# Kernel optimization log

Measured on AMD Instinct MI355X. Metric: run time of the kernel, lower is better.

## Reference

```python
import jax, jax.numpy as jnp
import numpy as np

B, S, H = 1, 2048, 2048
NH, HD, RD = 32, 64, 64      # n_heads, head_dim, qk_mqa_dim (rope dim)
QR, KVR = 1024, 896          # q_lora_rank, kv_lora_rank
EPS = 1e-6
SCALE = HD ** -0.5           # scaling = head_dim ** -0.5 (as in module)


def rotate_half(x):
    x1, x2 = jnp.split(x, 2, axis=-1)
    return jnp.concatenate((-x2, x1), axis=-1)


def rmsnorm(x, w):
    var = jnp.mean(jnp.square(x), axis=-1, keepdims=True)
    return x * jax.lax.rsqrt(var + EPS) * w


def setup_inputs() -> dict:
    key = jax.random.key(0)
    ks = jax.random.split(key, 8)
    hidden_states = jax.random.normal(ks[0], (B, S, H), jnp.float32)
    # rotary tables over RD dims (applied only to the rope slice)
    inv_freq = 1.0 / (10000.0 ** (np.arange(0, RD, 2, dtype=np.float32) / RD))
    ang = np.arange(S, dtype=np.float32)[:, None] * inv_freq[None, :]
    emb = np.concatenate([ang, ang], axis=-1)  # [S, RD]
    cos = jnp.tile(jnp.asarray(np.cos(emb))[None], (B, 1, 1))
    sin = jnp.tile(jnp.asarray(np.sin(emb))[None], (B, 1, 1))
    s = 0.02
    q_a_w = s * jax.random.normal(ks[1], (QR, H), jnp.float32)
    q_a_ln_w = jnp.ones((QR,), jnp.float32)
    q_b_w = s * jax.random.normal(ks[2], (NH * (HD + RD), QR), jnp.float32)
    kv_a_w = s * jax.random.normal(ks[3], (KVR + RD, H), jnp.float32)
    kv_a_ln_w = jnp.ones((KVR,), jnp.float32)
    kv_b_w = s * jax.random.normal(ks[4], (NH * 2 * HD, KVR), jnp.float32)
    o_w = s * jax.random.normal(ks[5], (H, NH * HD), jnp.float32)
    return {"hidden_states": hidden_states, "cos": cos, "sin": sin,
            "q_a_w": q_a_w, "q_a_ln_w": q_a_ln_w, "q_b_w": q_b_w,
            "kv_a_w": kv_a_w, "kv_a_ln_w": kv_a_ln_w, "kv_b_w": kv_b_w,
            "o_w": o_w}


def reference(hidden_states, cos, sin, q_a_w, q_a_ln_w, q_b_w,
              kv_a_w, kv_a_ln_w, kv_b_w, o_w):
    b, s, _ = hidden_states.shape
    # Q: low-rank down -> RMSNorm -> up, split nope/rope per head
    q_lat = rmsnorm(hidden_states @ q_a_w.T, q_a_ln_w)             # [B,S,QR]
    q = (q_lat @ q_b_w.T).reshape(b, s, NH, HD + RD).transpose(0, 2, 1, 3)
    q_nope, q_rope = q[..., :HD], q[..., HD:]                      # [B,NH,S,HD/RD]
    # KV: joint down-proj with shared MQA rope key
    ckv = hidden_states @ kv_a_w.T                                 # [B,S,KVR+RD]
    c_kv, k_rope = ckv[..., :KVR], ckv[..., KVR:]
    k_rope = k_rope[:, None]                                       # [B,1,S,RD]
    kv = (rmsnorm(c_kv, kv_a_ln_w) @ kv_b_w.T).reshape(b, s, NH, 2 * HD)
    kv = kv.transpose(0, 2, 1, 3)                                  # [B,NH,S,2HD]
    k_nope, v = kv[..., :HD], kv[..., HD:]
    # RoPE on rope slices only (cos/sin unsqueezed over head dim)
    c_, s_ = cos[:, None], sin[:, None]
    q_rope = q_rope * c_ + rotate_half(q_rope) * s_
    k_rope = k_rope * c_ + rotate_half(k_rope) * s_
    q_full = jnp.concatenate([q_nope, q_rope], axis=-1)            # [B,NH,S,HD+RD]
    k_full = jnp.concatenate(
        [k_nope, jnp.broadcast_to(k_rope, (b, NH, s, RD))], axis=-1)
    # causal SDPA
    scores = jnp.einsum('bhqd,bhkd->bhqk', q_full, k_full) * SCALE
    mask = jnp.tril(jnp.ones((s, s), bool))
    scores = jnp.where(mask, scores, jnp.finfo(scores.dtype).min)
    attn = jax.nn.softmax(scores, axis=-1)
    out = jnp.einsum('bhqk,bhkd->bhqd', attn, v)                   # [B,NH,S,HD]
    out = out.transpose(0, 2, 1, 3).reshape(b, s, NH * HD)
    return out @ o_w.T                                             # [B,S,H]
```

## Files before the change

kernel.cpp:

```cpp
#include <hip/hip_runtime.h>


typedef __attribute__((ext_vector_type(8))) __bf16 bf16x8;
typedef __attribute__((ext_vector_type(4))) float f32x4;
typedef __attribute__((ext_vector_type(4))) unsigned u32x4;

__device__ __forceinline__ unsigned short f2bf(float f) {
  unsigned int x = __builtin_bit_cast(unsigned int, f);
  x += 0x7fffu + ((x >> 16) & 1u);
  return (unsigned short)(x >> 16);
}
__device__ __forceinline__ float bf2f(unsigned short u) {
  unsigned int x = ((unsigned int)u) << 16;
  return __builtin_bit_cast(float, x);
}
__device__ __forceinline__ void gload_lds16(const void* g, void* l) {
  __builtin_amdgcn_global_load_lds(
      (const __attribute__((address_space(1))) void*)g,
      (__attribute__((address_space(3))) void*)l, 16, 0, 0);
}
__device__ __forceinline__ void cstore(float* C, size_t i, float v) { C[i] = v; }
__device__ __forceinline__ void cstore(unsigned short* C, size_t i, float v) { C[i] = f2bf(v); }

struct CvtSegs {
  const float* src[6];
  unsigned short* dst[6];
  unsigned int n_src[6];
  unsigned int n_tot[6];
  unsigned int blk0[7];
};

__global__ __launch_bounds__(256) void cvt_all(CvtSegs sg) {
  int b = blockIdx.x;
  int seg = 0;
#pragma unroll
  for (int k = 0; k < 5; ++k)
    if (b >= (int)sg.blk0[k + 1]) seg = k + 1;
  size_t i = ((size_t)(b - sg.blk0[seg]) * 256 + threadIdx.x) * 4;
  if (i >= sg.n_tot[seg]) return;
  unsigned short o0 = 0, o1 = 0, o2 = 0, o3 = 0;
  if (i < sg.n_src[seg]) {
    float4 v = *reinterpret_cast<const float4*>(sg.src[seg] + i);
    o0 = f2bf(v.x); o1 = f2bf(v.y); o2 = f2bf(v.z); o3 = f2bf(v.w);
  }
  *reinterpret_cast<ushort4*>(sg.dst[seg] + i) = make_ushort4(o0, o1, o2, o3);
}

template <typename OutT>
__global__ __launch_bounds__(512, 4) void gemm_bt2(const unsigned short* __restrict__ A,
                                                   const unsigned short* __restrict__ B,
                                                   OutT* __restrict__ C,
                                                   int M, int N, int K) {
  __shared__ unsigned short lA0[128 * 64], lA1[128 * 64];
  __shared__ unsigned short lB0[64 * 64], lB1[64 * 64];
  const int tid = threadIdx.x, lane = tid & 63, wv = tid >> 6;
  const int wr = wv >> 1, wc = wv & 1;

  unsigned nwg = gridDim.x * gridDim.y;
  unsigned lid = blockIdx.y * gridDim.x + blockIdx.x;
  unsigned swz_id = (lid & 7) * (nwg >> 3) + (lid >> 3);
  const int bm = (int)(swz_id / gridDim.x) * 128;
  const int bn = (int)(swz_id % gridDim.x) * 64;

  f32x4 acc[2][2] = {};

  const int ar0 = tid >> 3;
  const int acol = (((tid & 7) ^ ((tid >> 3) & 7))) * 8;
  const int swz = lane & 7;

  auto stage = [&](unsigned short* la, unsigned short* lb, int k0) {
#pragma unroll
    for (int i = 0; i < 2; ++i)
      gload_lds16(A + (size_t)(bm + i * 64 + ar0) * K + k0 + acol,
                  &la[(i * 512 + wv * 64) * 8]);
    gload_lds16(B + (size_t)(bn + ar0) * K + k0 + acol, &lb[(wv * 64) * 8]);
  };

  auto compute = [&](const unsigned short* la, const unsigned short* lb) {
#pragma unroll
    for (int ks = 0; ks < 2; ++ks) {
      const int ch = ((ks * 4 + (lane >> 4)) ^ swz) * 8;
      bf16x8 af[2], bfr[2];
#pragma unroll
      for (int m = 0; m < 2; ++m)
        af[m] = *reinterpret_cast<const bf16x8*>(
            &la[(wr * 32 + m * 16 + (lane & 15)) * 64 + ch]);
#pragma unroll
      for (int n = 0; n < 2; ++n)
        bfr[n] = *reinterpret_cast<const bf16x8*>(
            &lb[(wc * 32 + n * 16 + (lane & 15)) * 64 + ch]);
      __builtin_amdgcn_s_setprio(1);
#pragma unroll
      for (int m = 0; m < 2; ++m)
#pragma unroll
        for (int n = 0; n < 2; ++n)
          acc[m][n] = __builtin_amdgcn_mfma_f32_16x16x32_bf16(af[m], bfr[n], acc[m][n], 0, 0, 0);
      __builtin_amdgcn_s_setprio(0);
    }
  };

  stage(lA0, lB0, 0);
  for (int k0 = 0; k0 < K; k0 += 128) {
    __syncthreads();
    stage(lA1, lB1, k0 + 64);
    compute(lA0, lB0);
    __syncthreads();
    if (k0 + 128 < K) stage(lA0, lB0, k0 + 128);
    compute(lA1, lB1);
  }

  const int r0 = bm + wr * 32, c0 = bn + wc * 32;
#pragma unroll
  for (int m = 0; m < 2; ++m)
#pragma unroll
    for (int n = 0; n < 2; ++n)
#pragma unroll
      for (int r = 0; r < 4; ++r)
        cstore(C, (size_t)(r0 + m * 16 + (lane >> 4) * 4 + r) * N + c0 + n * 16 + (lane & 15),
               acc[m][n][r]);
}

__global__ __launch_bounds__(256) void rmsnorm_rope(const float* __restrict__ C1,
                                                    const float* __restrict__ qw,
                                                    const float* __restrict__ kvw,
                                                    const float* __restrict__ cosp,
                                                    const float* __restrict__ sinp,
                                                    unsigned short* __restrict__ qn,
                                                    unsigned short* __restrict__ ckvn,
                                                    unsigned short* __restrict__ kr) {
  const int s = blockIdx.x, tid = threadIdx.x;
  const float* row = C1 + (size_t)s * 2048;
  __shared__ float red[4];

  float4 v = *reinterpret_cast<const float4*>(row + tid * 4);
  float ss = v.x * v.x + v.y * v.y + v.z * v.z + v.w * v.w;
  ss += __shfl_xor(ss, 32); ss += __shfl_xor(ss, 16); ss += __shfl_xor(ss, 8);
  ss += __shfl_xor(ss, 4);  ss += __shfl_xor(ss, 2);  ss += __shfl_xor(ss, 1);
  if ((tid & 63) == 0) red[tid >> 6] = ss;
  __syncthreads();
  float rs = rsqrtf((red[0] + red[1] + red[2] + red[3]) * (1.f / 1024.f) + 1e-6f);
  {
    float4 w = *reinterpret_cast<const float4*>(qw + tid * 4);
    *reinterpret_cast<ushort4*>(qn + (size_t)s * 1024 + tid * 4) =
        make_ushort4(f2bf(v.x * rs * w.x), f2bf(v.y * rs * w.y),
                     f2bf(v.z * rs * w.z), f2bf(v.w * rs * w.w));
  }

  float4 u = make_float4(0.f, 0.f, 0.f, 0.f);
  if (tid < 224) u = *reinterpret_cast<const float4*>(row + 1024 + tid * 4);
  ss = u.x * u.x + u.y * u.y + u.z * u.z + u.w * u.w;
  ss += __shfl_xor(ss, 32); ss += __shfl_xor(ss, 16); ss += __shfl_xor(ss, 8);
  ss += __shfl_xor(ss, 4);  ss += __shfl_xor(ss, 2);  ss += __shfl_xor(ss, 1);
  __syncthreads();
  if ((tid & 63) == 0) red[tid >> 6] = ss;
  __syncthreads();
  rs = rsqrtf((red[0] + red[1] + red[2] + red[3]) * (1.f / 896.f) + 1e-6f);
  if (tid < 224) {
    float4 w = *reinterpret_cast<const float4*>(kvw + tid * 4);
    *reinterpret_cast<ushort4*>(ckvn + (size_t)s * 896 + tid * 4) =
        make_ushort4(f2bf(u.x * rs * w.x), f2bf(u.y * rs * w.y),
                     f2bf(u.z * rs * w.z), f2bf(u.w * rs * w.w));
  }

  if (tid < 64) {
    int d = tid;
    float x = row[1920 + d];
    float part = (d < 32) ? -row[1920 + d + 32] : row[1920 + d - 32];
    float vv = x * cosp[(size_t)s * 64 + d] + part * sinp[(size_t)s * 64 + d];
    kr[(size_t)s * 64 + d] = f2bf(vv);
  }
}

__global__ __launch_bounds__(256) void kv_post(const unsigned short* __restrict__ KVfb,
                                               unsigned short* __restrict__ Vt) {
  __shared__ unsigned short lT[64 * 65];
  const int s0 = blockIdx.x * 64, h = blockIdx.y, tid = threadIdx.x;
  for (int idx = tid; idx < 4096; idx += 256) {
    int r = idx >> 6, c = idx & 63;
    lT[r * 65 + c] = KVfb[(size_t)(s0 + r) * 4096 + h * 128 + 64 + c];
  }
  __syncthreads();
  for (int idx = tid; idx < 4096; idx += 256) {
    int d = idx >> 6, c = idx & 63;
    Vt[((size_t)h * 64 + d) * 2048 + s0 + c] = lT[c * 65 + d];
  }
}

__global__ __launch_bounds__(256, 4) void flash_attn(const unsigned short* __restrict__ Qfb,
                                                     const unsigned short* __restrict__ KVfb,
                                                     const unsigned short* __restrict__ kr,
                                                     const float* __restrict__ cosp,
                                                     const float* __restrict__ sinp,
                                                     const unsigned short* __restrict__ Vt,
                                                     float* __restrict__ Op,
                                                     float2* __restrict__ Ml) {
  __shared__ unsigned short lK0[64 * 128], lK1[64 * 128];
  const int tid = threadIdx.x, lane = tid & 63, wv = tid >> 6;
  const int h = blockIdx.x;
  const int qb = 31 - ((int)blockIdx.y >> 1);
  const int j = (int)blockIdx.y & 1;
  const int q0 = qb * 64;
  const int firstrow = q0 + wv * 16;
  const int g = lane >> 4;
  const int qa = firstrow + (lane & 15);
  const float SC = 0.18033688f;

  bf16x8 qf[4];
  {
    const unsigned short* qr = Qfb + (size_t)qa * 4096 + h * 128;
    float raw[4][8];
#pragma unroll
    for (int ks = 0; ks < 4; ++ks) {
      ushort4 u0 = *reinterpret_cast<const ushort4*>(qr + ks * 32 + g * 8);
      ushort4 u1 = *reinterpret_cast<const ushort4*>(qr + ks * 32 + g * 8 + 4);
      raw[ks][0] = bf2f(u0.x); raw[ks][1] = bf2f(u0.y);
      raw[ks][2] = bf2f(u0.z); raw[ks][3] = bf2f(u0.w);
      raw[ks][4] = bf2f(u1.x); raw[ks][5] = bf2f(u1.y);
      raw[ks][6] = bf2f(u1.z); raw[ks][7] = bf2f(u1.w);
    }
    const float* cp = cosp + (size_t)qa * 64 + g * 8;
    const float* sp = sinp + (size_t)qa * 64 + g * 8;
    float c0[8], s0[8], c1[8], s1[8];
    {
      float4 a = *reinterpret_cast<const float4*>(cp);
      float4 b = *reinterpret_cast<const float4*>(cp + 4);
      c0[0]=a.x;c0[1]=a.y;c0[2]=a.z;c0[3]=a.w;c0[4]=b.x;c0[5]=b.y;c0[6]=b.z;c0[7]=b.w;
      a = *reinterpret_cast<const float4*>(cp + 32);
      b = *reinterpret_cast<const float4*>(cp + 36);
      c1[0]=a.x;c1[1]=a.y;c1[2]=a.z;c1[3]=a.w;c1[4]=b.x;c1[5]=b.y;c1[6]=b.z;c1[7]=b.w;
      a = *reinterpret_cast<const float4*>(sp);
      b = *reinterpret_cast<const float4*>(sp + 4);
      s0[0]=a.x;s0[1]=a.y;s0[2]=a.z;s0[3]=a.w;s0[4]=b.x;s0[5]=b.y;s0[6]=b.z;s0[7]=b.w;
      a = *reinterpret_cast<const float4*>(sp + 32);
      b = *reinterpret_cast<const float4*>(sp + 36);
      s1[0]=a.x;s1[1]=a.y;s1[2]=a.z;s1[3]=a.w;s1[4]=b.x;s1[5]=b.y;s1[6]=b.z;s1[7]=b.w;
    }
    alignas(16) unsigned short pk[4][8];
#pragma unroll
    for (int e = 0; e < 8; ++e) {
      pk[0][e] = f2bf(raw[0][e] * SC);
      pk[1][e] = f2bf(raw[1][e] * SC);
      pk[2][e] = f2bf((raw[2][e] * c0[e] - raw[3][e] * s0[e]) * SC);
      pk[3][e] = f2bf((raw[3][e] * c1[e] + raw[2][e] * s1[e]) * SC);
    }
#pragma unroll
    for (int ks = 0; ks < 4; ++ks)
      qf[ks] = *reinterpret_cast<const bf16x8*>(pk[ks]);
  }

  f32x4 o_acc[4] = {};
  float mrow = -1e30f, lrow = 0.f;

  const int sl0 = ((g & 1) * 2) * 16 + (lane & 15);
  const int sl1 = sl0 + 16;
  const bool hi = g >= 2;

  const int krow = wv * 4 + (lane >> 4);
  const int cs = (lane & 15) ^ (krow & 7);
  const int swz = lane & 7;

  auto stage = [&](int t, unsigned short* lK) {
    int jj = t * 64;
#pragma unroll
    for (int i = 0; i < 4; ++i) {
      int s = jj + i * 16 + krow;
      const unsigned short* src =
          (cs < 8) ? KVfb + (size_t)s * 4096 + h * 128 + cs * 8
                   : kr + (size_t)s * 64 + (cs - 8) * 8;
      gload_lds16(src, &lK[(i * 16 + wv * 4) * 128]);
    }
  };

  auto loadV = [&](int j0, bf16x8 (&vr)[2][4]) {
#pragma unroll
    for (int ks = 0; ks < 2; ++ks)
#pragma unroll
      for (int n = 0; n < 4; ++n)
        vr[ks][n] = *reinterpret_cast<const bf16x8*>(
            Vt + ((size_t)h * 64 + n * 16 + (lane & 15)) * 2048 + j0 + ks * 32 +
            (lane >> 4) * 8);
  };

  auto computeT = [&](int j0, const unsigned short* lK, const bf16x8 (&vr)[2][4]) {
    f32x4 sT[4] = {};
    __builtin_amdgcn_s_setprio(1);
#pragma unroll
    for (int n = 0; n < 4; ++n)
#pragma unroll
      for (int ks = 0; ks < 4; ++ks) {
        bf16x8 kf = *reinterpret_cast<const bf16x8*>(
            &lK[(n * 16 + (lane & 15)) * 128 + (((ks * 4 + (lane >> 4)) ^ swz)) * 8]);
        sT[n] = __builtin_amdgcn_mfma_f32_16x16x32_bf16(kf, qf[ks], sT[n], 0, 0, 0);
      }
    __builtin_amdgcn_s_setprio(0);

    if (j0 == q0) {
#pragma unroll
      for (int n = 0; n < 4; ++n)
#pragma unroll
        for (int r = 0; r < 4; ++r) {
          int key = j0 + n * 16 + g * 4 + r;
          if (key > qa) sT[n][r] = -1e30f;
        }
    }

    float tm[4];
#pragma unroll
    for (int n = 0; n < 4; ++n)
      tm[n] = fmaxf(fmaxf(sT[n][0], sT[n][1]), fmaxf(sT[n][2], sT[n][3]));
    float mx = fmaxf(fmaxf(tm[0], tm[1]), fmaxf(tm[2], tm[3]));
    mx = fmaxf(mx, __shfl_xor(mx, 16));
    mx = fmaxf(mx, __shfl_xor(mx, 32));

    if (__any(mx - mrow > 8.0f)) {
      float mn = fmaxf(mrow, mx);
      float sf = exp2f(mrow - mn);
      mrow = mn;
      lrow *= sf;
      float sfr[4];
#pragma unroll
      for (int r = 0; r < 4; ++r) sfr[r] = __shfl(sf, (lane >> 4) * 4 + r);
#pragma unroll
      for (int n = 0; n < 4; ++n)
#pragma unroll
        for (int r = 0; r < 4; ++r) o_acc[n][r] *= sfr[r];
    }

    float psn[4];
    unsigned dw[4][2];
#pragma unroll
    for (int n = 0; n < 4; ++n) {
      float p0 = exp2f(sT[n][0] - mrow), p1 = exp2f(sT[n][1] - mrow);
      float p2 = exp2f(sT[n][2] - mrow), p3 = exp2f(sT[n][3] - mrow);
      psn[n] = (p0 + p1) + (p2 + p3);
      asm("v_cvt_pk_bf16_f32 %0, %1, %2" : "=v"(dw[n][0]) : "v"(p0), "v"(p1));
      asm("v_cvt_pk_bf16_f32 %0, %1, %2" : "=v"(dw[n][1]) : "v"(p2), "v"(p3));
    }
    float ps = (psn[0] + psn[1]) + (psn[2] + psn[3]);
    ps += __shfl_xor(ps, 16);
    ps += __shfl_xor(ps, 32);
    lrow += ps;

#pragma unroll
    for (int ks = 0; ks < 2; ++ks) {
      unsigned A0 = __shfl(dw[2 * ks][0], sl0);
      unsigned B0 = __shfl(dw[2 * ks + 1][0], sl0);
      unsigned A1 = __shfl(dw[2 * ks][1], sl0);
      unsigned B1 = __shfl(dw[2 * ks + 1][1], sl0);
      unsigned A2 = __shfl(dw[2 * ks][0], sl1);
      unsigned B2 = __shfl(dw[2 * ks + 1][0], sl1);
      unsigned A3 = __shfl(dw[2 * ks][1], sl1);
      unsigned B3 = __shfl(dw[2 * ks + 1][1], sl1);
      u32x4 mm;
      mm.x = hi ? B0 : A0; mm.y = hi ? B1 : A1;
      mm.z = hi ? B2 : A2; mm.w = hi ? B3 : A3;
      bf16x8 pa = __builtin_bit_cast(bf16x8, mm);
      __builtin_amdgcn_s_setprio(1);
#pragma unroll
      for (int n = 0; n < 4; ++n)
        o_acc[n] = __builtin_amdgcn_mfma_f32_16x16x32_bf16(pa, vr[ks][n], o_acc[n], 0, 0, 0);
      __builtin_amdgcn_s_setprio(0);
    }
  };

  bf16x8 vr[2][4];
  unsigned short* cur = lK0;
  unsigned short* nxt = lK1;
  if (j <= qb) stage(j, cur);
  for (int t = j; t <= qb; t += 2) {
    __syncthreads();
    if (t + 2 <= qb) stage(t + 2, nxt);
    loadV(t * 64, vr);
    computeT(t * 64, cur, vr);
    unsigned short* tmp = cur; cur = nxt; nxt = tmp;
  }

  float* op = Op + (size_t)j * 4194304 + ((size_t)h * 2048 + firstrow) * 64;
#pragma unroll
  for (int n = 0; n < 4; ++n)
#pragma unroll
    for (int r = 0; r < 4; ++r)
      op[(size_t)(g * 4 + r) * 64 + n * 16 + (lane & 15)] = o_acc[n][r];
  if (lane < 16)
    Ml[(size_t)j * 65536 + h * 2048 + qa] = make_float2(mrow, lrow);
}

__global__ __launch_bounds__(256) void flash_combine(const float* __restrict__ Op,
                                                     const float2* __restrict__ Ml,
                                                     unsigned short* __restrict__ Ao) {
  size_t i4 = ((size_t)blockIdx.x * 256 + threadIdx.x) * 4;
  int s = (int)(i4 >> 11);
  int c = (int)(i4 & 2047);
  int h = c >> 6, d = c & 63;
  float2 a = Ml[h * 2048 + s];
  float2 b = Ml[65536 + h * 2048 + s];
  float M = fmaxf(a.x, b.x);
  float w0 = exp2f(a.x - M), w1 = exp2f(b.x - M);
  float inv = 1.f / (w0 * a.y + w1 * b.y);
  size_t pidx = ((size_t)h * 2048 + s) * 64 + d;
  float4 o0 = *reinterpret_cast<const float4*>(Op + pidx);
  float4 o1 = *reinterpret_cast<const float4*>(Op + 4194304 + pidx);
  *reinterpret_cast<ushort4*>(Ao + (size_t)s * 2048 + h * 64 + d) =
      make_ushort4(f2bf((w0 * o0.x + w1 * o1.x) * inv),
                   f2bf((w0 * o0.y + w1 * o1.y) * inv),
                   f2bf((w0 * o0.z + w1 * o1.z) * inv),
                   f2bf((w0 * o0.w + w1 * o1.w) * inv));
}

extern "C" void kernel_launch(void* const* d_in, const int* in_sizes, int n_in,
                              void* d_out, int out_size, void* d_ws, size_t ws_size,
                              hipStream_t stream) {
  const float* hs   = (const float*)d_in[0];
  const float* cosp = (const float*)d_in[1];
  const float* sinp = (const float*)d_in[2];
  const float* qaw  = (const float*)d_in[3];
  const float* qaln = (const float*)d_in[4];
  const float* qbwf = (const float*)d_in[5];
  const float* kvaw = (const float*)d_in[6];
  const float* kvln = (const float*)d_in[7];
  const float* kvbwf= (const float*)d_in[8];
  const float* owf  = (const float*)d_in[9];
  float* out = (float*)d_out;
  char* ws = (char*)d_ws;
  const size_t MB = 1u << 20;

  unsigned short* W1b  = (unsigned short*)(ws + 0);
  unsigned short* Ao   = (unsigned short*)(ws + 0);
  unsigned short* qbw  = (unsigned short*)(ws + 8 * MB);
  unsigned short* Vt   = (unsigned short*)(ws + 8 * MB);
  unsigned short* kvbw = (unsigned short*)(ws + 16 * MB);
  unsigned short* owb  = (unsigned short*)(ws + 23 * MB);
  unsigned short* hsb  = (unsigned short*)(ws + 31 * MB);
  unsigned short* Qfb  = (unsigned short*)(ws + 31 * MB);
  float*          C1   = (float*)(ws + 47 * MB);
  unsigned short* KVfb = (unsigned short*)(ws + 63 * MB);
  unsigned short* kr   = (unsigned short*)(ws + 79 * MB);
  unsigned short* qln  = (unsigned short*)(ws + 80 * MB);
  unsigned short* ckvn = (unsigned short*)(ws + 84 * MB);
  float*          Op   = (float*)(ws + 88 * MB);
  float2*         Mlp  = (float2*)(ws + 122 * MB);
  (void)ws_size; (void)in_sizes; (void)n_in; (void)out_size;

  CvtSegs sg;
  sg.src[0] = qaw;   sg.dst[0] = W1b;                      sg.n_src[0] = 1024u * 2048u; sg.n_tot[0] = 1024u * 2048u;
  sg.src[1] = kvaw;  sg.dst[1] = W1b + (size_t)1024 * 2048; sg.n_src[1] = 960u * 2048u;  sg.n_tot[1] = 1024u * 2048u;
  sg.src[2] = hs;    sg.dst[2] = hsb;                      sg.n_src[2] = 2048u * 2048u; sg.n_tot[2] = 2048u * 2048u;
  sg.src[3] = qbwf;  sg.dst[3] = qbw;                      sg.n_src[3] = 4096u * 1024u; sg.n_tot[3] = 4096u * 1024u;
  sg.src[4] = kvbwf; sg.dst[4] = kvbw;                     sg.n_src[4] = 4096u * 896u;  sg.n_tot[4] = 4096u * 896u;
  sg.src[5] = owf;   sg.dst[5] = owb;                      sg.n_src[5] = 2048u * 2048u; sg.n_tot[5] = 2048u * 2048u;
  sg.blk0[0] = 0;
  for (int k = 0; k < 6; ++k) sg.blk0[k + 1] = sg.blk0[k] + sg.n_tot[k] / 1024u;
  cvt_all<<<dim3(sg.blk0[6]), 256, 0, stream>>>(sg);

  gemm_bt2<float><<<dim3(32, 16), 512, 0, stream>>>(hsb, W1b, C1, 2048, 2048, 2048);
  rmsnorm_rope<<<2048, 256, 0, stream>>>(C1, qaln, kvln, cosp, sinp, qln, ckvn, kr);
  gemm_bt2<unsigned short><<<dim3(64, 16), 512, 0, stream>>>(qln, qbw, Qfb, 2048, 4096, 1024);
  gemm_bt2<unsigned short><<<dim3(64, 16), 512, 0, stream>>>(ckvn, kvbw, KVfb, 2048, 4096, 896);

  kv_post<<<dim3(32, 32), 256, 0, stream>>>(KVfb, Vt);

  flash_attn<<<dim3(32, 64), 256, 0, stream>>>(Qfb, KVfb, kr, cosp, sinp, Vt, Op, Mlp);
  flash_combine<<<dim3(4096), 256, 0, stream>>>(Op, Mlp, Ao);

  gemm_bt2<float><<<dim3(32, 16), 512, 0, stream>>>(Ao, owb, out, 2048, 2048, 2048);
}
```

Measured before the change: 221.0 us.

## Merge Q and KV up-projection GEMMs into one launch; raise flash_attn occupancy hint

The GEMM body is factored into a device function, and a new paired kernel runs the q_b and kv_b up-projection GEMMs as two halves of a single 2048-block grid. This removes one kernel launch and the tail/idle gap between two back-to-back 1024-block GEMMs, letting both fill the GPU together. Separately, flash_attn's launch bounds minimum blocks per CU goes from 4 to 5, which may force fewer registers and risk spills.

```diff
diff --git a/kernel.cpp b/kernel.cpp
--- a/kernel.cpp
+++ b/kernel.cpp
@@ -47,20 +47,14 @@
 }
 
 template <typename OutT>
-__global__ __launch_bounds__(512, 4) void gemm_bt2(const unsigned short* __restrict__ A,
-                                                   const unsigned short* __restrict__ B,
-                                                   OutT* __restrict__ C,
-                                                   int M, int N, int K) {
-  __shared__ unsigned short lA0[128 * 64], lA1[128 * 64];
-  __shared__ unsigned short lB0[64 * 64], lB1[64 * 64];
+__device__ __forceinline__ void gemm_body(const unsigned short* __restrict__ A,
+                                          const unsigned short* __restrict__ B,
+                                          OutT* __restrict__ C,
+                                          int N, int K, int bm, int bn,
+                                          unsigned short* lA0, unsigned short* lA1,
+                                          unsigned short* lB0, unsigned short* lB1) {
   const int tid = threadIdx.x, lane = tid & 63, wv = tid >> 6;
   const int wr = wv >> 1, wc = wv & 1;
-
-  unsigned nwg = gridDim.x * gridDim.y;
-  unsigned lid = blockIdx.y * gridDim.x + blockIdx.x;
-  unsigned swz_id = (lid & 7) * (nwg >> 3) + (lid >> 3);
-  const int bm = (int)(swz_id / gridDim.x) * 128;
-  const int bn = (int)(swz_id % gridDim.x) * 64;
 
   f32x4 acc[2][2] = {};
 
@@ -118,6 +112,42 @@
       for (int r = 0; r < 4; ++r)
         cstore(C, (size_t)(r0 + m * 16 + (lane >> 4) * 4 + r) * N + c0 + n * 16 + (lane & 15),
                acc[m][n][r]);
+}
+
+template <typename OutT>
+__global__ __launch_bounds__(512, 4) void gemm_bt2(const unsigned short* __restrict__ A,
+                                                   const unsigned short* __restrict__ B,
+                                                   OutT* __restrict__ C,
+                                                   int M, int N, int K) {
+  __shared__ unsigned short lA0[128 * 64], lA1[128 * 64];
+  __shared__ unsigned short lB0[64 * 64], lB1[64 * 64];
+  unsigned nwg = gridDim.x * gridDim.y;
+  unsigned lid = blockIdx.y * gridDim.x + blockIdx.x;
+  unsigned swz_id = (lid & 7) * (nwg >> 3) + (lid >> 3);
+  const int bm = (int)(swz_id / gridDim.x) * 128;
+  const int bn = (int)(swz_id % gridDim.x) * 64;
+  gemm_body<OutT>(A, B, C, N, K, bm, bn, lA0, lA1, lB0, lB1);
+}
+
+__global__ __launch_bounds__(512, 4) void gemm_bt2_pair(const unsigned short* __restrict__ A0,
+                                                        const unsigned short* __restrict__ B0,
+                                                        unsigned short* __restrict__ C0,
+                                                        int K0,
+                                                        const unsigned short* __restrict__ A1,
+                                                        const unsigned short* __restrict__ B1,
+                                                        unsigned short* __restrict__ C1,
+                                                        int K1) {
+  __shared__ unsigned short lA0[128 * 64], lA1[128 * 64];
+  __shared__ unsigned short lB0[64 * 64], lB1[64 * 64];
+  const int p = blockIdx.x >= 1024;
+  unsigned lid = blockIdx.x & 1023;
+  unsigned swz_id = (lid & 7) * 128 + (lid >> 3);
+  const int bm = (int)(swz_id >> 6) * 128;
+  const int bn = (int)(swz_id & 63) * 64;
+  if (!p)
+    gemm_body<unsigned short>(A0, B0, C0, 4096, K0, bm, bn, lA0, lA1, lB0, lB1);
+  else
+    gemm_body<unsigned short>(A1, B1, C1, 4096, K1, bm, bn, lA0, lA1, lB0, lB1);
 }
 
 __global__ __launch_bounds__(256) void rmsnorm_rope(const float* __restrict__ C1,
@@ -186,7 +216,7 @@
   }
 }
 
-__global__ __launch_bounds__(256, 4) void flash_attn(const unsigned short* __restrict__ Qfb,
+__global__ __launch_bounds__(256, 5) void flash_attn(const unsigned short* __restrict__ Qfb,
                                                      const unsigned short* __restrict__ KVfb,
                                                      const unsigned short* __restrict__ kr,
                                                      const float* __restrict__ cosp,
@@ -454,8 +484,9 @@
 
   gemm_bt2<float><<<dim3(32, 16), 512, 0, stream>>>(hsb, W1b, C1, 2048, 2048, 2048);
   rmsnorm_rope<<<2048, 256, 0, stream>>>(C1, qaln, kvln, cosp, sinp, qln, ckvn, kr);
-  gemm_bt2<unsigned short><<<dim3(64, 16), 512, 0, stream>>>(qln, qbw, Qfb, 2048, 4096, 1024);
-  gemm_bt2<unsigned short><<<dim3(64, 16), 512, 0, stream>>>(ckvn, kvbw, KVfb, 2048, 4096, 896);
+
+  gemm_bt2_pair<<<dim3(2048), 512, 0, stream>>>(qln, qbw, Qfb, 1024,
+                                                ckvn, kvbw, KVfb, 896);
 
   kv_post<<<dim3(32, 32), 256, 0, stream>>>(KVfb, Vt);
 
```

After: 272.6 us. 1.23x slower.
